# Optimization experiments

Measured on AMD Instinct MI355X. Metric: run time of the kernel, lower is better.

## Reference

```python
import jax, jax.numpy as jnp
import numpy as np

N_BINS = 20  # matches init kwarg n_bins


def setup_inputs() -> dict:
    key = jax.random.key(0)
    k1, k2 = jax.random.split(key)
    preds = jax.random.uniform(k1, (16, 1024, 1024), dtype=jnp.float32)
    targets = jax.random.uniform(k2, (16, 1024, 1024), dtype=jnp.float32)
    return {"preds": preds, "targets": targets}


def reference(preds, targets):
    # Single-pass scatter histogram replacing the original per-bin mask loop.
    p = preds.reshape(-1)
    t = targets.reshape(-1).astype(jnp.float32)
    # torch loop: element belongs to bin i iff bins[i] <= p < bins[i+1];
    # p outside [0,1) (e.g. exactly 1.0) falls in no bin.
    idx = jnp.clip(jnp.floor(p * N_BINS).astype(jnp.int32), 0, N_BINS - 1)
    w = ((p >= 0.0) & (p < 1.0)).astype(p.dtype)  # in-range indicator (constant wrt grads)
    cnt = jax.ops.segment_sum(w, idx, num_segments=N_BINS)           # per-bin counts
    sum_p = jax.ops.segment_sum(p * w, idx, num_segments=N_BINS)     # per-bin sum of confidences
    sum_t = jax.ops.segment_sum(t * w, idx, num_segments=N_BINS)     # per-bin sum of accuracies
    valid = cnt > 0
    safe_cnt = jnp.where(valid, cnt, 1.0)
    per_bin = jnp.abs(sum_p / safe_cnt - sum_t / safe_cnt)
    n_valid = jnp.sum(valid.astype(p.dtype))
    ace = jnp.sum(jnp.where(valid, per_bin, 0.0)) / jnp.maximum(n_valid, 1.0)
    return ace
```

## Files before the change

kernel.cpp:

```cpp
#include <hip/hip_runtime.h>

#define NBINS 20
#define NQ (3 * NBINS)
#define BT 128

__global__ __launch_bounds__(BT) void ace_partial(
    const float4* __restrict__ preds4, const float4* __restrict__ targs4,
    const float* __restrict__ preds, const float* __restrict__ targs,
    float* __restrict__ gsums, int nvec, int n)
{
    __shared__ float hist[NQ * BT];
    const int tid = threadIdx.x;

    #pragma unroll
    for (int q = 0; q < NQ; ++q)
        hist[q * BT + tid] = 0.0f;
    __syncthreads();

    float* hc = &hist[(0 * NBINS) * BT + tid];
    float* hp = &hist[(1 * NBINS) * BT + tid];
    float* ht = &hist[(2 * NBINS) * BT + tid];

    const int stride = gridDim.x * BT;
    int i = blockIdx.x * BT + tid;

    if (i < nvec) {
        float4 pa = preds4[i];
        float4 ta = targs4[i];
        for (;;) {
            const int j = i + stride;
            const bool hasNext = j < nvec;
            float4 pb, tb;
            if (hasNext) { pb = preds4[j]; tb = targs4[j]; }

            const float pv[4] = {pa.x, pa.y, pa.z, pa.w};
            const float tv[4] = {ta.x, ta.y, ta.z, ta.w};
            #pragma unroll
            for (int e = 0; e < 4; ++e) {
                const float p = pv[e];
                int b = (int)(p * (float)NBINS);
                b = b < 0 ? 0 : (b > NBINS - 1 ? NBINS - 1 : b);
                const float w = (p >= 0.0f && p < 1.0f) ? 1.0f : 0.0f;
                const int o = b * BT;
                hc[o] += w;
                hp[o] += p * w;
                ht[o] += tv[e] * w;
            }

            if (!hasNext) break;
            pa = pb; ta = tb; i = j;
        }
    }

    if (blockIdx.x == 0 && tid == 0) {
        for (int r = nvec * 4; r < n; ++r) {
            const float p = preds[r];
            int b = (int)(p * (float)NBINS);
            b = b < 0 ? 0 : (b > NBINS - 1 ? NBINS - 1 : b);
            const float w = (p >= 0.0f && p < 1.0f) ? 1.0f : 0.0f;
            const int o = b * BT;
            hc[o] += w;
            hp[o] += p * w;
            ht[o] += targs[r] * w;
        }
    }

    #pragma unroll
    for (int s = BT / 2; s >= 1; s >>= 1) {
        __syncthreads();
        for (int k = tid; k < NQ * s; k += BT) {
            const int q = k / s, c = k - q * s;
            hist[q * BT + c] += hist[q * BT + c + s];
        }
    }
    __syncthreads();

    if (tid < NQ)
        atomicAdd(&gsums[tid], hist[tid * BT]);
}

__global__ __launch_bounds__(64) void ace_final(
    const float* __restrict__ gsums, float* __restrict__ out)
{
    const int l = threadIdx.x;
    float per = 0.0f, valid = 0.0f;
    if (l < NBINS) {
        const float cnt = gsums[l];
        const float sp  = gsums[NBINS + l];
        const float st  = gsums[2 * NBINS + l];
        if (cnt > 0.0f) {
            valid = 1.0f;
            per = fabsf(sp / cnt - st / cnt);
        }
    }
    #pragma unroll
    for (int off = 32; off; off >>= 1) {
        per   += __shfl_down(per, off);
        valid += __shfl_down(valid, off);
    }
    if (l == 0)
        out[0] = per / fmaxf(valid, 1.0f);
}

extern "C" void kernel_launch(void* const* d_in, const int* in_sizes, int n_in,
                              void* d_out, int out_size, void* d_ws, size_t ws_size,
                              hipStream_t stream)
{
    const float* preds = (const float*)d_in[0];
    const float* targs = (const float*)d_in[1];
    const int n = in_sizes[0];
    const int nvec = n / 4;

    float* gsums = (float*)d_ws;
    hipMemsetAsync(gsums, 0, NQ * sizeof(float), stream);

    const int nblocks = 1280;
    ace_partial<<<nblocks, BT, 0, stream>>>(
        (const float4*)preds, (const float4*)targs, preds, targs,
        gsums, nvec, n);
    ace_final<<<1, 64, 0, stream>>>(gsums, (float*)d_out);
}
```

Before: 173.0 us.

## Replace shared-memory per-thread histograms with register accumulators and wave shuffles

Each thread now keeps its 20-bin count, confidence and accuracy sums in registers. Every element is compared against every bin and added with a predicated multiply-add, which replaces the dynamically indexed LDS read-modify-write per element. The block reduction becomes a wavefront xor-shuffle followed by a small shared-memory combine across waves, replacing the log-step LDS tree with its many barriers. Block size and grid size are also adjusted. The trade is about 60 extra VALU ops per element and higher register pressure, in exchange for removing LDS latency and bank traffic from the hot loop.

```diff
diff --git a/kernel.cpp b/kernel.cpp
--- a/kernel.cpp
+++ b/kernel.cpp
@@ -2,31 +2,23 @@
 
 #define NBINS 20
 #define NQ (3 * NBINS)
-#define BT 128
+#define BT 256
 
-__global__ __launch_bounds__(BT) void ace_partial(
+__global__ __launch_bounds__(BT, 4) void ace_partial(
     const float4* __restrict__ preds4, const float4* __restrict__ targs4,
     const float* __restrict__ preds, const float* __restrict__ targs,
     float* __restrict__ gsums, int nvec, int n)
 {
-    __shared__ float hist[NQ * BT];
+    float cacc[NBINS], pacc[NBINS], tacc[NBINS];
+    #pragma unroll
+    for (int b = 0; b < NBINS; ++b) { cacc[b] = 0.f; pacc[b] = 0.f; tacc[b] = 0.f; }
+
     const int tid = threadIdx.x;
-
-    #pragma unroll
-    for (int q = 0; q < NQ; ++q)
-        hist[q * BT + tid] = 0.0f;
-    __syncthreads();
-
-    float* hc = &hist[(0 * NBINS) * BT + tid];
-    float* hp = &hist[(1 * NBINS) * BT + tid];
-    float* ht = &hist[(2 * NBINS) * BT + tid];
-
     const int stride = gridDim.x * BT;
     int i = blockIdx.x * BT + tid;
 
     if (i < nvec) {
-        float4 pa = preds4[i];
-        float4 ta = targs4[i];
+        float4 pa = preds4[i], ta = targs4[i];
         for (;;) {
             const int j = i + stride;
             const bool hasNext = j < nvec;
@@ -38,15 +30,17 @@
             #pragma unroll
             for (int e = 0; e < 4; ++e) {
                 const float p = pv[e];
-                int b = (int)(p * (float)NBINS);
-                b = b < 0 ? 0 : (b > NBINS - 1 ? NBINS - 1 : b);
-                const float w = (p >= 0.0f && p < 1.0f) ? 1.0f : 0.0f;
-                const int o = b * BT;
-                hc[o] += w;
-                hp[o] += p * w;
-                ht[o] += tv[e] * w;
+                const float t = tv[e];
+                float fidx = floorf(p * (float)NBINS);
+                if (!(p >= 0.0f && p < 1.0f)) fidx = -1.0f;
+                #pragma unroll
+                for (int b = 0; b < NBINS; ++b) {
+                    const float m = (fidx == (float)b) ? 1.0f : 0.0f;
+                    cacc[b] += m;
+                    pacc[b] = fmaf(m, p, pacc[b]);
+                    tacc[b] = fmaf(m, t, tacc[b]);
+                }
             }
-
             if (!hasNext) break;
             pa = pb; ta = tb; i = j;
         }
@@ -55,28 +49,46 @@
     if (blockIdx.x == 0 && tid == 0) {
         for (int r = nvec * 4; r < n; ++r) {
             const float p = preds[r];
-            int b = (int)(p * (float)NBINS);
-            b = b < 0 ? 0 : (b > NBINS - 1 ? NBINS - 1 : b);
-            const float w = (p >= 0.0f && p < 1.0f) ? 1.0f : 0.0f;
-            const int o = b * BT;
-            hc[o] += w;
-            hp[o] += p * w;
-            ht[o] += targs[r] * w;
+            const float t = targs[r];
+            float fidx = floorf(p * (float)NBINS);
+            if (!(p >= 0.0f && p < 1.0f)) fidx = -1.0f;
+            #pragma unroll
+            for (int b = 0; b < NBINS; ++b) {
+                const float m = (fidx == (float)b) ? 1.0f : 0.0f;
+                cacc[b] += m;
+                pacc[b] = fmaf(m, p, pacc[b]);
+                tacc[b] = fmaf(m, t, tacc[b]);
+            }
         }
     }
 
     #pragma unroll
-    for (int s = BT / 2; s >= 1; s >>= 1) {
-        __syncthreads();
-        for (int k = tid; k < NQ * s; k += BT) {
-            const int q = k / s, c = k - q * s;
-            hist[q * BT + c] += hist[q * BT + c + s];
+    for (int b = 0; b < NBINS; ++b) {
+        #pragma unroll
+        for (int off = 32; off; off >>= 1) {
+            cacc[b] += __shfl_xor(cacc[b], off);
+            pacc[b] += __shfl_xor(pacc[b], off);
+            tacc[b] += __shfl_xor(tacc[b], off);
+        }
+    }
+
+    __shared__ float red[NQ][BT / 64];
+    const int wv = tid >> 6;
+    if ((tid & 63) == 0) {
+        #pragma unroll
+        for (int b = 0; b < NBINS; ++b) {
+            red[b][wv]             = cacc[b];
+            red[NBINS + b][wv]     = pacc[b];
+            red[2 * NBINS + b][wv] = tacc[b];
         }
     }
     __syncthreads();
-
-    if (tid < NQ)
-        atomicAdd(&gsums[tid], hist[tid * BT]);
+    if (tid < NQ) {
+        float s = 0.f;
+        #pragma unroll
+        for (int w = 0; w < BT / 64; ++w) s += red[tid][w];
+        atomicAdd(&gsums[tid], s);
+    }
 }
 
 __global__ __launch_bounds__(64) void ace_final(
@@ -114,7 +126,7 @@
     float* gsums = (float*)d_ws;
     hipMemsetAsync(gsums, 0, NQ * sizeof(float), stream);
 
-    const int nblocks = 1280;
+    const int nblocks = 1024;
     ace_partial<<<nblocks, BT, 0, stream>>>(
         (const float4*)preds, (const float4*)targs, preds, targs,
         gsums, nvec, n);
```

Measured after the change: 166.6 us. -3.7%, faster.
